# Optimization experiments

Hardware: AMD Instinct MI355X
Metric: run time of the kernel (lower is better)

The kernel has to match this reference:

```python
import jax, jax.numpy as jnp
import numpy as np

N_NODES = 100000
N_EDGES = 3200000
N_RELS = 8
F_IN = 64
F_OUT = 64


def setup_inputs() -> dict:
    key = jax.random.key(0)
    k1, k2, k3, k4, k5, k6 = jax.random.split(key, 6)
    X = jax.random.normal(k1, (N_NODES, F_IN), dtype=jnp.float32)
    W = jax.random.normal(k2, (N_RELS, F_IN, F_OUT), dtype=jnp.float32) * 0.1
    A = jax.random.uniform(k3, (N_EDGES,), dtype=jnp.float32)
    src = jax.random.randint(k4, (N_EDGES,), 0, N_NODES, dtype=jnp.int32)
    dst = jax.random.randint(k5, (N_EDGES,), 0, N_NODES, dtype=jnp.int32)
    etype = jax.random.randint(k6, (N_EDGES,), 0, N_RELS, dtype=jnp.int32)
    return {"X": X, "W": W, "A": A, "src": src, "dst": dst, "etype": etype}


def reference(X, W, A, src, dst, etype):
    # RGCN hetero forward: Y[i,fo] = sum_{r,j in N_r(i)} A[r,i,j] * (X[j] @ W[r])[fo]
    # Precompute per-relation transformed features: [R, N, F_out]
    XW = jnp.einsum('nf,rfo->rno', X, W)
    # Gather per-edge message and scale by edge weight: [E, F_out]
    msg = XW[etype, src] * A[:, None]
    # Scatter-add into destination nodes: [N, F_out]
    Y = jax.ops.segment_sum(msg, dst, num_segments=X.shape[0])
    return Y
```

## Files before the change

kernel.cpp:

```cpp
#include <hip/hip_runtime.h>
#include <hip/hip_fp16.h>

#define FDIM 64
#define P_BLK 1024
#define NB_MAX 800
#define BKT_NODES 128
#define CHUNK_CAP 3200
#define SEG_PAD 5120
#define SEG_CAP 4608
#define OVF_CAP 64

typedef __attribute__((ext_vector_type(8))) short short8;
typedef __attribute__((ext_vector_type(4))) float float4_;

__device__ __forceinline__ unsigned short f2bf(float x) {
    unsigned u = __float_as_uint(x);
    return (unsigned short)((u + 0x7FFF + ((u >> 16) & 1)) >> 16);
}

__global__ __launch_bounds__(256) void xw_gemm_mfma(
    const float* __restrict__ X, const float* __restrict__ Wmat,
    __half* __restrict__ XWh, int N, int R)
{
    __shared__ unsigned short Wt[4 * 64 * 72];
    __shared__ unsigned short Ot[4][16 * 72];
    const int tid  = threadIdx.x;
    const int lane = tid & 63;
    const int wave = tid >> 6;
    const int quad = lane >> 4;
    const int l15  = lane & 15;
    const int blockBase = blockIdx.x * 256;

    short8 bfrag[4][2];
    bool tvalid[4];
#pragma unroll
    for (int t = 0; t < 4; ++t) {
        const int tb = blockBase + (wave * 4 + t) * 16;
        tvalid[t] = (tb < N);
        if (tvalid[t]) {
            const float* xp = X + (size_t)(tb + l15) * FDIM + quad * 8;
            const float4 x0 = *(const float4*)(xp);
            const float4 x1 = *(const float4*)(xp + 4);
            const float4 x2 = *(const float4*)(xp + 32);
            const float4 x3 = *(const float4*)(xp + 36);
            short8 b0, b1;
            b0[0]=f2bf(x0.x); b0[1]=f2bf(x0.y); b0[2]=f2bf(x0.z); b0[3]=f2bf(x0.w);
            b0[4]=f2bf(x1.x); b0[5]=f2bf(x1.y); b0[6]=f2bf(x1.z); b0[7]=f2bf(x1.w);
            b1[0]=f2bf(x2.x); b1[1]=f2bf(x2.y); b1[2]=f2bf(x2.z); b1[3]=f2bf(x2.w);
            b1[4]=f2bf(x3.x); b1[5]=f2bf(x3.y); b1[6]=f2bf(x3.z); b1[7]=f2bf(x3.w);
            bfrag[t][0] = b0; bfrag[t][1] = b1;
        } else {
            bfrag[t][0] = (short8)(0); bfrag[t][1] = (short8)(0);
        }
    }

    for (int rp = 0; rp < 2; ++rp) {
        __syncthreads();
#pragma unroll
        for (int it = 0; it < 16; ++it) {
            const int idx = it * 256 + tid;
            const int k  = idx & 63;
            const int f4 = (idx >> 6) & 15;
            const int r  = idx >> 10;
            const float4 w = *(const float4*)(Wmat + (((size_t)(rp * 4 + r) * FDIM + k) * FDIM + f4 * 4));
            const int base = (r * 64 + f4 * 4) * 72 + k;
            Wt[base + 0 * 72] = f2bf(w.x);
            Wt[base + 1 * 72] = f2bf(w.y);
            Wt[base + 2 * 72] = f2bf(w.z);
            Wt[base + 3 * 72] = f2bf(w.w);
        }
        __syncthreads();

#pragma unroll
        for (int t = 0; t < 4; ++t) {
            if (!tvalid[t]) continue;
            const int tb = blockBase + (wave * 4 + t) * 16;
#pragma unroll
            for (int r = 0; r < 4; ++r) {
#pragma unroll
                for (int ft = 0; ft < 4; ++ft) {
                    const int f = ft * 16 + l15;
                    const unsigned short* wp = &Wt[(r * 64 + f) * 72 + quad * 8];
                    const short8 a0 = *(const short8*)(wp);
                    const short8 a1 = *(const short8*)(wp + 32);
                    float4_ acc = {0.f, 0.f, 0.f, 0.f};
                    acc = __builtin_amdgcn_mfma_f32_16x16x32_bf16(a0, bfrag[t][0], acc, 0, 0, 0);
                    acc = __builtin_amdgcn_mfma_f32_16x16x32_bf16(a1, bfrag[t][1], acc, 0, 0, 0);
                    const __half2 h01 = __floats2half2_rn(acc[0], acc[1]);
                    const __half2 h23 = __floats2half2_rn(acc[2], acc[3]);
                    uint2 st;
                    st.x = *(const unsigned*)&h01;
                    st.y = *(const unsigned*)&h23;
                    *(uint2*)&Ot[wave][l15 * 72 + ft * 16 + quad * 4] = st;
                }
                const int node = lane >> 2;
                const int c    = lane & 3;
                const uint4 w0 = *(const uint4*)&Ot[wave][node * 72 + c * 16];
                const uint4 w1 = *(const uint4*)&Ot[wave][node * 72 + c * 16 + 8];
                __half* orow = XWh + ((size_t)(rp * 4 + r) * N + (tb + node)) * FDIM;
                *(uint4*)(orow + c * 16)     = w0;
                *(uint4*)(orow + c * 16 + 8) = w1;
            }
        }
    }
}

__global__ __launch_bounds__(1024) void init_cursors(int* __restrict__ gcur, int B)
{
    const int b = (int)(blockIdx.x * 1024 + threadIdx.x);
    if (b < B) gcur[b] = b * SEG_PAD;
}

__global__ __launch_bounds__(256) void bin_scatter(
    const int* __restrict__ src, const int* __restrict__ dst,
    const int* __restrict__ etype, const float* __restrict__ A,
    int* __restrict__ gcur, int2* __restrict__ packed,
    int E, int N, int B, int chunk)
{
    __shared__ int lcnt[NB_MAX];
    __shared__ int lpfx[NB_MAX];
    __shared__ int gb[NB_MAX];
    __shared__ int2 recs[CHUNK_CAP];
    __shared__ unsigned short rbkt[CHUNK_CAP];
    const int p = blockIdx.x, tid = threadIdx.x;
    const int i0 = p * chunk, iend = min(i0 + chunk, E);

    for (int b = tid; b < B; b += 256) lcnt[b] = 0;
    __syncthreads();
    for (int i = i0 + tid; i < iend; i += 256)
        atomicAdd(&lcnt[dst[i] >> 7], 1);
    __syncthreads();

    if (tid < 64) {
        int carry = 0;
        for (int t0 = 0; t0 < B; t0 += 64) {
            const int b = t0 + tid;
            const int c = (b < B) ? lcnt[b] : 0;
            int v = c;
#pragma unroll
            for (int o = 1; o < 64; o <<= 1) {
                const int u = __shfl_up(v, o, 64);
                if (tid >= o) v += u;
            }
            if (b < B) lpfx[b] = carry + v - c;
            carry += __shfl(v, 63, 64);
        }
    }
    __syncthreads();
    for (int b = tid; b < B; b += 256) {
        const int c = lcnt[b];
        const int rbase = c ? atomicAdd(&gcur[b], c) : 0;
        gb[b] = rbase - lpfx[b];
        lcnt[b] = lpfx[b];
    }
    __syncthreads();

    for (int i = i0 + tid; i < iend; i += 256) {
        const int d = dst[i];
        const int b = d >> 7;
        const int slot = atomicAdd(&lcnt[b], 1);
        recs[slot] = make_int2((etype[i] * N + src[i]) | ((d & 127) << 20),
                               __float_as_int(A[i]));
        rbkt[slot] = (unsigned short)b;
    }
    __syncthreads();

    const int tot = iend - i0;
    for (int s = tid; s < tot; s += 256)
        packed[gb[rbkt[s]] + s] = recs[s];
}

__global__ __launch_bounds__(512) void agg_fused(
    const __half* __restrict__ XWh, const int2* __restrict__ packed,
    const int* __restrict__ gcur, float* __restrict__ Y, int N)
{
    __shared__ int2 recs[SEG_CAP];
    __shared__ int hist[BKT_NODES];
    __shared__ int pfx[BKT_NODES + 1];
    __shared__ int cur[BKT_NODES];
    __shared__ int2 ovf[OVF_CAP];
    __shared__ int ovfN;
    const int bkt = blockIdx.x, tid = threadIdx.x;
    const int segBase = bkt * SEG_PAD;
    const int cnt = gcur[bkt] - segBase;

    if (tid < BKT_NODES) hist[tid] = 0;
    if (tid == 0) ovfN = 0;
    __syncthreads();
    for (int i = tid; i < cnt; i += 512)
        atomicAdd(&hist[(packed[segBase + i].x >> 20) & 127], 1);
    __syncthreads();
    if (tid < 64) {
        int carry = 0;
#pragma unroll
        for (int t0 = 0; t0 < BKT_NODES; t0 += 64) {
            const int b = t0 + tid;
            const int c = hist[b];
            int v = c;
#pragma unroll
            for (int o = 1; o < 64; o <<= 1) {
                const int u = __shfl_up(v, o, 64);
                if (tid >= o) v += u;
            }
            pfx[b] = carry + v - c;
            cur[b] = carry + v - c;
            carry += __shfl(v, 63, 64);
            if (tid == 0 && t0 + 64 == BKT_NODES) pfx[BKT_NODES] = carry;
        }
    }
    __syncthreads();
    for (int i = tid; i < cnt; i += 512) {
        const int2 rec = packed[segBase + i];
        const int dl = (rec.x >> 20) & 127;
        const int pos = atomicAdd(&cur[dl], 1);
        if (pos < SEG_CAP) recs[pos] = rec;
        else { const int o = atomicAdd(&ovfN, 1); if (o < OVF_CAP) ovf[o] = rec; }
    }
    __syncthreads();

    const int lane = tid & 63;
    const int w    = tid >> 6;
    const int el   = lane >> 4;
    const int fl4  = lane & 15;
    const __half2* __restrict__ XW2 = (const __half2*)XWh;
    const unsigned foff = (unsigned)(fl4 << 1);

    for (int j = 0; j < 16; ++j) {
        const int nl = w * 16 + j;
        const int gnode = bkt * BKT_NODES + nl;
        if (gnode >= N) break;
        const int beg = min(pfx[nl], SEG_CAP);
        const int end = min(pfx[nl + 1], SEG_CAP);
        float4_ acc = {0.f, 0.f, 0.f, 0.f};
        for (int b2 = beg; b2 < end; b2 += 64) {
            const int idx = b2 + lane;
            const int2 ka = (idx < end) ? recs[idx] : make_int2(0, 0);
            const int nb = min(64, end - b2);
            const int nsteps = (((nb + 3) >> 2) + 7) & ~7;
            for (int s = 0; s < nsteps; s += 8) {
                int k[8], bv[8];
#pragma unroll
                for (int u = 0; u < 8; ++u) {
                    const int jj = ((s + u) << 2) + el;
                    k[u]  = __shfl(ka.x, jj, 64);
                    bv[u] = __shfl(ka.y, jj, 64);
                }
                uint2 v[8];
#pragma unroll
                for (int u = 0; u < 8; ++u)
                    v[u] = *(const uint2*)(XW2 + ((((unsigned)k[u]) & 0xFFFFFu) << 5) + foff);
#pragma unroll
                for (int u = 0; u < 8; ++u) {
                    const float a = __int_as_float(bv[u]);
                    const float2 f0 = __half22float2(*(const __half2*)&v[u].x);
                    const float2 f1 = __half22float2(*(const __half2*)&v[u].y);
                    acc[0] += a * f0.x; acc[1] += a * f0.y;
                    acc[2] += a * f1.x; acc[3] += a * f1.y;
                }
            }
        }
#pragma unroll
        for (int m = 16; m <= 32; m <<= 1) {
            acc[0] += __shfl_xor(acc[0], m, 64);
            acc[1] += __shfl_xor(acc[1], m, 64);
            acc[2] += __shfl_xor(acc[2], m, 64);
            acc[3] += __shfl_xor(acc[3], m, 64);
        }
        if (lane < 16)
            *(float4_*)(Y + (size_t)gnode * FDIM + (fl4 << 2)) = acc;
    }
    __syncthreads();

    const int no = min(ovfN, OVF_CAP);
    for (int o = tid; o < no; o += 512) {
        const int2 rec = ovf[o];
        const int node = bkt * BKT_NODES + ((rec.x >> 20) & 127);
        if (node < N) {
            const float a = __int_as_float(rec.y);
            const __half* row = XWh + (size_t)(rec.x & 0xFFFFF) * FDIM;
            for (int f = 0; f < FDIM; ++f)
                atomicAdd(&Y[(size_t)node * FDIM + f], a * __half2float(row[f]));
        }
    }
}

extern "C" void kernel_launch(void* const* d_in, const int* in_sizes, int n_in,
                              void* d_out, int out_size, void* d_ws, size_t ws_size,
                              hipStream_t stream)
{
    const float* X     = (const float*)d_in[0];
    const float* Wmat  = (const float*)d_in[1];
    const float* A     = (const float*)d_in[2];
    const int*   src   = (const int*)d_in[3];
    const int*   dst   = (const int*)d_in[4];
    const int*   etype = (const int*)d_in[5];
    float* Y = (float*)d_out;

    const int N = in_sizes[0] / FDIM;
    const int R = in_sizes[1] / (FDIM * FDIM);
    const int E = in_sizes[2];
    (void)n_in; (void)out_size; (void)ws_size;

    const int B = (N + BKT_NODES - 1) / BKT_NODES;
    const int chunk = (E + P_BLK - 1) / P_BLK;

    char* ws = (char*)d_ws;
    size_t off = 0;
    auto take = [&](size_t bytes) { char* p = ws + off; off = (off + bytes + 255) & ~(size_t)255; return p; };
    __half* XWh    = (__half*)take((size_t)R * N * FDIM * sizeof(__half));
    int2*   packed = (int2*)  take((size_t)B * SEG_PAD * sizeof(int2));
    int*    gcur   = (int*)   take((size_t)B * sizeof(int));

    init_cursors<<<1, 1024, 0, stream>>>(gcur, B);
    xw_gemm_mfma<<<(N + 255) / 256, 256, 0, stream>>>(X, Wmat, XWh, N, R);
    bin_scatter<<<P_BLK, 256, 0, stream>>>(src, dst, etype, A, gcur, packed, E, N, B, chunk);
    agg_fused<<<B, 512, 0, stream>>>(XWh, packed, gcur, Y, N);
}
```

Before: 303.1 us.

## Split edge binning into two-level coarse/fine radix scatter and parallelize GEMM over relations

Result: faster. 291.9 us (-3.7%).

```diff
diff --git a/kernel.cpp b/kernel.cpp
--- a/kernel.cpp
+++ b/kernel.cpp
@@ -3,12 +3,18 @@
 
 #define FDIM 64
 #define P_BLK 1024
+#define NSB_MAX 32
+#define SB_BITS 12
+#define SB_PAD 135168
+#define CHUNK_CAP 3200
+#define CHUNK2 4224
+#define SPB 32
 #define NB_MAX 800
 #define BKT_NODES 128
-#define CHUNK_CAP 3200
-#define SEG_PAD 5120
+#define SEG_PAD 4608
 #define SEG_CAP 4608
 #define OVF_CAP 64
+#define CUR_STRIDE 16
 
 typedef __attribute__((ext_vector_type(8))) short short8;
 typedef __attribute__((ext_vector_type(4))) float float4_;
@@ -29,6 +35,7 @@
     const int wave = tid >> 6;
     const int quad = lane >> 4;
     const int l15  = lane & 15;
+    const int rp   = blockIdx.y;
     const int blockBase = blockIdx.x * 256;
 
     short8 bfrag[4][2];
@@ -54,120 +61,179 @@
         }
     }
 
-    for (int rp = 0; rp < 2; ++rp) {
-        __syncthreads();
-#pragma unroll
-        for (int it = 0; it < 16; ++it) {
-            const int idx = it * 256 + tid;
-            const int k  = idx & 63;
-            const int f4 = (idx >> 6) & 15;
-            const int r  = idx >> 10;
-            const float4 w = *(const float4*)(Wmat + (((size_t)(rp * 4 + r) * FDIM + k) * FDIM + f4 * 4));
-            const int base = (r * 64 + f4 * 4) * 72 + k;
-            Wt[base + 0 * 72] = f2bf(w.x);
-            Wt[base + 1 * 72] = f2bf(w.y);
-            Wt[base + 2 * 72] = f2bf(w.z);
-            Wt[base + 3 * 72] = f2bf(w.w);
-        }
-        __syncthreads();
-
-#pragma unroll
-        for (int t = 0; t < 4; ++t) {
-            if (!tvalid[t]) continue;
-            const int tb = blockBase + (wave * 4 + t) * 16;
-#pragma unroll
-            for (int r = 0; r < 4; ++r) {
-#pragma unroll
-                for (int ft = 0; ft < 4; ++ft) {
-                    const int f = ft * 16 + l15;
-                    const unsigned short* wp = &Wt[(r * 64 + f) * 72 + quad * 8];
-                    const short8 a0 = *(const short8*)(wp);
-                    const short8 a1 = *(const short8*)(wp + 32);
-                    float4_ acc = {0.f, 0.f, 0.f, 0.f};
-                    acc = __builtin_amdgcn_mfma_f32_16x16x32_bf16(a0, bfrag[t][0], acc, 0, 0, 0);
-                    acc = __builtin_amdgcn_mfma_f32_16x16x32_bf16(a1, bfrag[t][1], acc, 0, 0, 0);
-                    const __half2 h01 = __floats2half2_rn(acc[0], acc[1]);
-                    const __half2 h23 = __floats2half2_rn(acc[2], acc[3]);
-                    uint2 st;
-                    st.x = *(const unsigned*)&h01;
-                    st.y = *(const unsigned*)&h23;
-                    *(uint2*)&Ot[wave][l15 * 72 + ft * 16 + quad * 4] = st;
-                }
-                const int node = lane >> 2;
-                const int c    = lane & 3;
-                const uint4 w0 = *(const uint4*)&Ot[wave][node * 72 + c * 16];
-                const uint4 w1 = *(const uint4*)&Ot[wave][node * 72 + c * 16 + 8];
-                __half* orow = XWh + ((size_t)(rp * 4 + r) * N + (tb + node)) * FDIM;
-                *(uint4*)(orow + c * 16)     = w0;
-                *(uint4*)(orow + c * 16 + 8) = w1;
+#pragma unroll
+    for (int it = 0; it < 16; ++it) {
+        const int idx = it * 256 + tid;
+        const int k  = idx & 63;
+        const int f4 = (idx >> 6) & 15;
+        const int r  = idx >> 10;
+        const float4 w = *(const float4*)(Wmat + (((size_t)(rp * 4 + r) * FDIM + k) * FDIM + f4 * 4));
+        const int base = (r * 64 + f4 * 4) * 72 + k;
+        Wt[base + 0 * 72] = f2bf(w.x);
+        Wt[base + 1 * 72] = f2bf(w.y);
+        Wt[base + 2 * 72] = f2bf(w.z);
+        Wt[base + 3 * 72] = f2bf(w.w);
+    }
+    __syncthreads();
+
+#pragma unroll
+    for (int t = 0; t < 4; ++t) {
+        if (!tvalid[t]) continue;
+        const int tb = blockBase + (wave * 4 + t) * 16;
+#pragma unroll
+        for (int r = 0; r < 4; ++r) {
+#pragma unroll
+            for (int ft = 0; ft < 4; ++ft) {
+                const int f = ft * 16 + l15;
+                const unsigned short* wp = &Wt[(r * 64 + f) * 72 + quad * 8];
+                const short8 a0 = *(const short8*)(wp);
+                const short8 a1 = *(const short8*)(wp + 32);
+                float4_ acc = {0.f, 0.f, 0.f, 0.f};
+                acc = __builtin_amdgcn_mfma_f32_16x16x32_bf16(a0, bfrag[t][0], acc, 0, 0, 0);
+                acc = __builtin_amdgcn_mfma_f32_16x16x32_bf16(a1, bfrag[t][1], acc, 0, 0, 0);
+                const __half2 h01 = __floats2half2_rn(acc[0], acc[1]);
+                const __half2 h23 = __floats2half2_rn(acc[2], acc[3]);
+                uint2 st;
+                st.x = *(const unsigned*)&h01;
+                st.y = *(const unsigned*)&h23;
+                *(uint2*)&Ot[wave][l15 * 72 + ft * 16 + quad * 4] = st;
             }
-        }
-    }
-}
-
-__global__ __launch_bounds__(1024) void init_cursors(int* __restrict__ gcur, int B)
-{
-    const int b = (int)(blockIdx.x * 1024 + threadIdx.x);
-    if (b < B) gcur[b] = b * SEG_PAD;
-}
-
-__global__ __launch_bounds__(256) void bin_scatter(
+            const int node = lane >> 2;
+            const int c    = lane & 3;
+            const uint4 w0 = *(const uint4*)&Ot[wave][node * 72 + c * 16];
+            const uint4 w1 = *(const uint4*)&Ot[wave][node * 72 + c * 16 + 8];
+            __half* orow = XWh + ((size_t)(rp * 4 + r) * N + (tb + node)) * FDIM;
+            *(uint4*)(orow + c * 16)     = w0;
+            *(uint4*)(orow + c * 16 + 8) = w1;
+        }
+    }
+}
+
+__global__ __launch_bounds__(1024) void init_cursors(
+    int* __restrict__ gcur1, int* __restrict__ gcur2, int NSB, int B)
+{
+    const int t = (int)(blockIdx.x * 1024 + threadIdx.x);
+    if (t < NSB) gcur1[t * CUR_STRIDE] = t * SB_PAD;
+    if (t < B)   gcur2[t * CUR_STRIDE] = t * SEG_PAD;
+}
+
+__global__ __launch_bounds__(256) void scatter_coarse(
     const int* __restrict__ src, const int* __restrict__ dst,
     const int* __restrict__ etype, const float* __restrict__ A,
-    int* __restrict__ gcur, int2* __restrict__ packed,
-    int E, int N, int B, int chunk)
-{
-    __shared__ int lcnt[NB_MAX];
-    __shared__ int lpfx[NB_MAX];
-    __shared__ int gb[NB_MAX];
+    int* __restrict__ gcur1, int2* __restrict__ packed1,
+    int E, int N, int NSB, int chunk)
+{
+    __shared__ int lcnt[NSB_MAX];
+    __shared__ int gb[NSB_MAX];
     __shared__ int2 recs[CHUNK_CAP];
-    __shared__ unsigned short rbkt[CHUNK_CAP];
+    __shared__ unsigned char rbkt[CHUNK_CAP];
     const int p = blockIdx.x, tid = threadIdx.x;
     const int i0 = p * chunk, iend = min(i0 + chunk, E);
 
-    for (int b = tid; b < B; b += 256) lcnt[b] = 0;
+    if (tid < NSB_MAX) lcnt[tid] = 0;
     __syncthreads();
     for (int i = i0 + tid; i < iend; i += 256)
-        atomicAdd(&lcnt[dst[i] >> 7], 1);
+        atomicAdd(&lcnt[dst[i] >> SB_BITS], 1);
     __syncthreads();
 
     if (tid < 64) {
-        int carry = 0;
-        for (int t0 = 0; t0 < B; t0 += 64) {
-            const int b = t0 + tid;
-            const int c = (b < B) ? lcnt[b] : 0;
-            int v = c;
-#pragma unroll
-            for (int o = 1; o < 64; o <<= 1) {
-                const int u = __shfl_up(v, o, 64);
-                if (tid >= o) v += u;
-            }
-            if (b < B) lpfx[b] = carry + v - c;
-            carry += __shfl(v, 63, 64);
-        }
-    }
-    __syncthreads();
-    for (int b = tid; b < B; b += 256) {
-        const int c = lcnt[b];
-        const int rbase = c ? atomicAdd(&gcur[b], c) : 0;
-        gb[b] = rbase - lpfx[b];
-        lcnt[b] = lpfx[b];
+        const int c = (tid < NSB) ? lcnt[tid] : 0;
+        int v = c;
+#pragma unroll
+        for (int o = 1; o < 64; o <<= 1) {
+            const int u = __shfl_up(v, o, 64);
+            if (tid >= o) v += u;
+        }
+        if (tid < NSB) gb[tid] = v - c;
+    }
+    __syncthreads();
+    if (tid < NSB) {
+        const int c = lcnt[tid];
+        const int pfx = gb[tid];
+        const int rbase = c ? atomicAdd(&gcur1[tid * CUR_STRIDE], c) : 0;
+        gb[tid] = rbase - pfx;
+        lcnt[tid] = pfx;
     }
     __syncthreads();
 
     for (int i = i0 + tid; i < iend; i += 256) {
         const int d = dst[i];
-        const int b = d >> 7;
-        const int slot = atomicAdd(&lcnt[b], 1);
-        recs[slot] = make_int2((etype[i] * N + src[i]) | ((d & 127) << 20),
+        const int sb = d >> SB_BITS;
+        const int slot = atomicAdd(&lcnt[sb], 1);
+        recs[slot] = make_int2((etype[i] * N + src[i]) | ((d & 127) << 20) | (((d >> 7) & 31) << 27),
                                __float_as_int(A[i]));
-        rbkt[slot] = (unsigned short)b;
+        rbkt[slot] = (unsigned char)sb;
     }
     __syncthreads();
 
     const int tot = iend - i0;
-    for (int s = tid; s < tot; s += 256)
-        packed[gb[rbkt[s]] + s] = recs[s];
+    for (int s = tid; s < tot; s += 256) {
+        const int b = rbkt[s];
+        const int gi = gb[b] + s;
+        if (gi < (b + 1) * SB_PAD)
+            packed1[gi] = recs[s];
+    }
+}
+
+__global__ __launch_bounds__(256) void scatter_fine(
+    const int2* __restrict__ packed1, const int* __restrict__ gcur1,
+    int* __restrict__ gcur2, int2* __restrict__ packed2, int B)
+{
+    __shared__ int lcnt[32];
+    __shared__ int gb[32];
+    __shared__ int2 recs[CHUNK2];
+    __shared__ unsigned char rbkt[CHUNK2];
+    const int sb  = (int)blockIdx.x >> 5;
+    const int cix = (int)blockIdx.x & 31;
+    const int tid = threadIdx.x;
+    const int sbBase = sb * SB_PAD;
+    const int sbCnt = min(gcur1[sb * CUR_STRIDE] - sbBase, SB_PAD);
+    const int i0 = cix * CHUNK2, iend = min(i0 + CHUNK2, sbCnt);
+    if (i0 >= sbCnt) return;
+
+    if (tid < 32) lcnt[tid] = 0;
+    __syncthreads();
+    for (int i = i0 + tid; i < iend; i += 256)
+        atomicAdd(&lcnt[(packed1[sbBase + i].x >> 27) & 31], 1);
+    __syncthreads();
+
+    if (tid < 64) {
+        const int c = (tid < 32) ? lcnt[tid] : 0;
+        int v = c;
+#pragma unroll
+        for (int o = 1; o < 64; o <<= 1) {
+            const int u = __shfl_up(v, o, 64);
+            if (tid >= o) v += u;
+        }
+        if (tid < 32) gb[tid] = v - c;
+    }
+    __syncthreads();
+    if (tid < 32) {
+        const int bglob = sb * 32 + tid;
+        const int c = lcnt[tid];
+        const int pfx = gb[tid];
+        const int rbase = (c && bglob < B) ? atomicAdd(&gcur2[bglob * CUR_STRIDE], c) : 0;
+        gb[tid] = rbase - pfx;
+        lcnt[tid] = pfx;
+    }
+    __syncthreads();
+
+    for (int i = i0 + tid; i < iend; i += 256) {
+        const int2 rec = packed1[sbBase + i];
+        const int fb = (rec.x >> 27) & 31;
+        const int slot = atomicAdd(&lcnt[fb], 1);
+        recs[slot] = rec;
+        rbkt[slot] = (unsigned char)fb;
+    }
+    __syncthreads();
+
+    const int tot = iend - i0;
+    for (int s = tid; s < tot; s += 256) {
+        const int fb = rbkt[s];
+        const int gi = gb[fb] + s;
+        if (gi < (sb * 32 + fb + 1) * SEG_PAD)
+            packed2[gi] = recs[s];
+    }
 }
 
 __global__ __launch_bounds__(512) void agg_fused(
@@ -182,7 +248,7 @@
     __shared__ int ovfN;
     const int bkt = blockIdx.x, tid = threadIdx.x;
     const int segBase = bkt * SEG_PAD;
-    const int cnt = gcur[bkt] - segBase;
+    const int cnt = min(gcur[bkt * CUR_STRIDE] - segBase, SEG_PAD);
 
     if (tid < BKT_NODES) hist[tid] = 0;
     if (tid == 0) ovfN = 0;
@@ -301,18 +367,22 @@
     const int E = in_sizes[2];
     (void)n_in; (void)out_size; (void)ws_size;
 
-    const int B = (N + BKT_NODES - 1) / BKT_NODES;
+    const int B   = (N + BKT_NODES - 1) / BKT_NODES;
+    const int NSB = (N + (1 << SB_BITS) - 1) >> SB_BITS;
     const int chunk = (E + P_BLK - 1) / P_BLK;
 
     char* ws = (char*)d_ws;
     size_t off = 0;
     auto take = [&](size_t bytes) { char* p = ws + off; off = (off + bytes + 255) & ~(size_t)255; return p; };
-    __half* XWh    = (__half*)take((size_t)R * N * FDIM * sizeof(__half));
-    int2*   packed = (int2*)  take((size_t)B * SEG_PAD * sizeof(int2));
-    int*    gcur   = (int*)   take((size_t)B * sizeof(int));
-
-    init_cursors<<<1, 1024, 0, stream>>>(gcur, B);
-    xw_gemm_mfma<<<(N + 255) / 256, 256, 0, stream>>>(X, Wmat, XWh, N, R);
-    bin_scatter<<<P_BLK, 256, 0, stream>>>(src, dst, etype, A, gcur, packed, E, N, B, chunk);
-    agg_fused<<<B, 512, 0, stream>>>(XWh, packed, gcur, Y, N);
-}
+    __half* XWh     = (__half*)take((size_t)R * N * FDIM * sizeof(__half));
+    int2*   packed1 = (int2*)  take((size_t)NSB * SB_PAD * sizeof(int2));
+    int2*   packed2 = (int2*)  take((size_t)B * SEG_PAD * sizeof(int2));
+    int*    gcur1   = (int*)   take((size_t)NSB * CUR_STRIDE * sizeof(int));
+    int*    gcur2   = (int*)   take((size_t)B * CUR_STRIDE * sizeof(int));
+
+    init_cursors<<<1, 1024, 0, stream>>>(gcur1, gcur2, NSB, B);
+    xw_gemm_mfma<<<dim3((N + 255) / 256, (R + 3) / 4), 256, 0, stream>>>(X, Wmat, XWh, N, R);
+    scatter_coarse<<<P_BLK, 256, 0, stream>>>(src, dst, etype, A, gcur1, packed1, E, N, NSB, chunk);
+    scatter_fine<<<NSB * SPB, 256, 0, stream>>>(packed1, gcur1, gcur2, packed2, B);
+    agg_fused<<<B, 512, 0, stream>>>(XWh, packed2, gcur2, Y, N);
+}
```
